# Kernel optimization log

Hardware: AMD Instinct MI355X
Metric: run time of the kernel (lower is better)

Reference implementation:

```python
import jax, jax.numpy as jnp
import numpy as np

ROWS, COLS = 4096, 8192
K = 4096                      # target_mask_size (<= COLS)
TEMPERATURE = 2.0 / 3.0


def setup_inputs() -> dict:
    key = jax.random.key(0)
    k1, k2 = jax.random.split(key)
    # param_init_fn: normal(mean=log(1-0.5)-log(0.5)=0, std=0.01)
    z_loga = jax.random.normal(k1, (ROWS, COLS), dtype=jnp.float32) * 0.01
    # eps = rand_like(...).clamp_(1e-6, 1-1e-6)
    eps = jax.random.uniform(k2, (ROWS, COLS), dtype=jnp.float32,
                             minval=1e-6, maxval=1.0 - 1e-6)
    return {"z_loga": z_loga, "eps": eps, "step": 0}


def reference(z_loga, eps, step):
    # Training branch of Mask.sample_z: gumbel-sigmoid + per-row top-k hard mask
    # with straight-through estimator.
    gumbel = -jnp.log(-jnp.log(eps))                       # [R, C]
    gumbel_mask = jax.nn.sigmoid((z_loga + gumbel) / TEMPERATURE)
    # per-row top-k hard selection (dim=1), scatter ones at top-k indices
    _, idx = jax.lax.top_k(gumbel_mask, K)                 # [R, K]
    rows = jnp.arange(gumbel_mask.shape[0])[:, None]       # [R, 1]
    hard = jnp.zeros_like(gumbel_mask).at[rows, idx].set(1.0)
    # straight-through: forward = hard, gradient flows through gumbel_mask
    st = hard - jax.lax.stop_gradient(gumbel_mask) + gumbel_mask
    return st.reshape(ROWS, COLS)                          # mask_output_shape
```

## Files before the change

kernel.cpp:

```cpp
#include <hip/hip_runtime.h>
#include <math.h>
#include <stdint.h>

#define ROWS 4096
#define COLS 8192
#define KSEL 4096
#define NT 256
#define NWAVE (NT / 64)
#define PT (COLS / (4 * NT))
#define NBINS 1024
#define WMAX 128
#define RANGE_HI 0.75f
#define LN2F 0.69314718056f

__device__ __forceinline__ int bin_of(float u) {
    int b = (int)(u * ((float)NBINS / RANGE_HI));
    b = b < 0 ? 0 : b;
    b = b > NBINS - 1 ? NBINS - 1 : b;
    return b;
}

__global__ __launch_bounds__(NT) void mask_topk_kernel(
    const float* __restrict__ z, const float* __restrict__ eps,
    float* __restrict__ out)
{
    __shared__ uint32_t hist[NWAVE][NBINS];
    __shared__ uint32_t wtot[NWAVE];
    __shared__ int      winIdx[WMAX];
    __shared__ uint32_t winSig[WMAX];
    __shared__ int      s_B, s_need2;
    __shared__ uint32_t s_wcount;

    const int row  = blockIdx.x;
    const int tid  = threadIdx.x;
    const int lane = tid & 63;
    const int wave = tid >> 6;
    const size_t rbase = (size_t)row * COLS;

    const float4* z4 = (const float4*)(z + rbase);
    const float4* e4 = (const float4*)(eps + rbase);
    float4 zr[PT], er[PT];
#pragma unroll
    for (int it = 0; it < PT; ++it) {
        zr[it] = z4[it * NT + tid];
        er[it] = e4[it * NT + tid];
    }

    for (int i = tid; i < NWAVE * NBINS; i += NT) ((uint32_t*)hist)[i] = 0;
    if (tid == 0) s_wcount = 0;
    __syncthreads();

    uint32_t cLo = 0, cHi = 0;
#pragma unroll
    for (int it = 0; it < PT; ++it) {
        float zz[4] = {zr[it].x, zr[it].y, zr[it].z, zr[it].w};
        float ee[4] = {er[it].x, er[it].y, er[it].z, er[it].w};
        float uu[4];
#pragma unroll
        for (int j = 0; j < 4; ++j) {
            float l1 = __builtin_amdgcn_logf(ee[j]) * LN2F;
            float l2 = __builtin_amdgcn_logf(-l1) * LN2F;
            uu[j] = zz[j] - l2;
            int b = bin_of(uu[j]);
            if (b == 0)              ++cLo;
            else if (b == NBINS - 1) ++cHi;
            else atomicAdd(&hist[wave][b], 1u);
        }
        zr[it].x = uu[0]; zr[it].y = uu[1]; zr[it].z = uu[2]; zr[it].w = uu[3];
    }
#pragma unroll
    for (int off = 32; off >= 1; off >>= 1) {
        cLo += __shfl_down(cLo, off, 64);
        cHi += __shfl_down(cHi, off, 64);
    }
    if (lane == 0) {
        atomicAdd(&hist[wave][0],         cLo);
        atomicAdd(&hist[wave][NBINS - 1], cHi);
    }
    __syncthreads();

    const int hb = tid * (NBINS / NT);
    uint32_t h[NBINS / NT];
    uint32_t cs = 0;
#pragma unroll
    for (int i = 0; i < NBINS / NT; ++i) {
        uint32_t t = 0;
#pragma unroll
        for (int c = 0; c < NWAVE; ++c) t += hist[c][hb + i];
        h[i] = t;
        cs += t;
    }
    uint32_t v = cs;
#pragma unroll
    for (int off = 1; off < 64; off <<= 1) {
        uint32_t t = __shfl_down(v, off, 64);
        if (lane + off < 64) v += t;
    }
    if (lane == 0) wtot[wave] = v;
    __syncthreads();
    uint32_t above = 0;
#pragma unroll
    for (int c = 0; c < NWAVE; ++c) above += (c > wave) ? wtot[c] : 0u;
    uint32_t cum = (v + above) - cs;

    for (int i = NBINS / NT - 1; i >= 0; --i) {
        if (cum < KSEL && KSEL <= cum + h[i]) {
            const int Bq = hb + i;
            uint32_t hB1 = 0;
            if (Bq + 1 < NBINS) {
#pragma unroll
                for (int c = 0; c < NWAVE; ++c) hB1 += hist[c][Bq + 1];
            }
            s_B = Bq;
            s_need2 = KSEL - (int)(cum - hB1);
        }
        cum += h[i];
    }
    __syncthreads();
    const int B = s_B;
    const int need2 = s_need2;

    float4* o4 = (float4*)(out + rbase);
#pragma unroll
    for (int it = 0; it < PT; ++it) {
        const int k = it * NT + tid;
        float uu[4] = {zr[it].x, zr[it].y, zr[it].z, zr[it].w};
        float oo[4];
#pragma unroll
        for (int j = 0; j < 4; ++j) {
            int b = bin_of(uu[j]);
            oo[j] = (b > B + 1) ? 1.0f : 0.0f;
            if (b >= B - 1 && b <= B + 1) {
                uint32_t slot = atomicAdd(&s_wcount, 1u);
                if (slot < WMAX) {
                    const int idx = k * 4 + j;
                    winIdx[slot] = idx;
                    float e   = eps[rbase + idx];
                    float zz  = z[rbase + idx];
                    float l1  = (float)log((double)e);
                    float l2  = (float)log((double)(-l1));
                    float g   = -l2;
                    float s   = zz + g;
                    float t   = s / (2.0f / 3.0f);
                    float ex  = (float)exp(-(double)t);
                    float sig = 1.0f / (1.0f + ex);
                    winSig[slot] = __float_as_uint(sig);
                }
            }
        }
        float4 ov; ov.x = oo[0]; ov.y = oo[1]; ov.z = oo[2]; ov.w = oo[3];
        o4[k] = ov;
    }
    __syncthreads();

    int w = (int)s_wcount; if (w > WMAX) w = WMAX;
    if (tid < 64) {
        for (int j = lane; j < w; j += 64) {
            uint32_t sj = winSig[j];
            int ij = winIdx[j];
            int rank = 0;
            for (int kk = 0; kk < w; ++kk) {
                uint32_t sk = winSig[kk];
                int ik = winIdx[kk];
                rank += (sk > sj || (sk == sj && ik < ij)) ? 1 : 0;
            }
            out[rbase + ij] = (rank < need2) ? 1.0f : 0.0f;
        }
    }
}

extern "C" void kernel_launch(void* const* d_in, const int* in_sizes, int n_in,
                              void* d_out, int out_size, void* d_ws, size_t ws_size,
                              hipStream_t stream) {
    const float* z   = (const float*)d_in[0];
    const float* eps = (const float*)d_in[1];
    float* out = (float*)d_out;
    hipLaunchKernelGGL(mask_topk_kernel, dim3(ROWS), dim3(NT), 0, stream,
                       z, eps, out);
}
```

Baseline: 322.8 us.

## Process one row per wavefront and keep packed bin indices in registers

```diff
diff --git a/kernel.cpp b/kernel.cpp
--- a/kernel.cpp
+++ b/kernel.cpp
@@ -7,11 +7,14 @@
 #define KSEL 4096
 #define NT 256
 #define NWAVE (NT / 64)
-#define PT (COLS / (4 * NT))
+#define NIT (COLS / (4 * 64))
 #define NBINS 1024
+#define BPL (NBINS / 64)
 #define WMAX 128
 #define RANGE_HI 0.75f
 #define LN2F 0.69314718056f
+
+typedef float fvec4 __attribute__((ext_vector_type(4)));
 
 __device__ __forceinline__ int bin_of(float u) {
     int b = (int)(u * ((float)NBINS / RANGE_HI));
@@ -20,53 +23,50 @@
     return b;
 }
 
-__global__ __launch_bounds__(NT) void mask_topk_kernel(
+__global__ __launch_bounds__(NT, 2) void mask_topk_kernel(
     const float* __restrict__ z, const float* __restrict__ eps,
     float* __restrict__ out)
 {
     __shared__ uint32_t hist[NWAVE][NBINS];
-    __shared__ uint32_t wtot[NWAVE];
-    __shared__ int      winIdx[WMAX];
-    __shared__ uint32_t winSig[WMAX];
-    __shared__ int      s_B, s_need2;
-    __shared__ uint32_t s_wcount;
+    __shared__ int      winIdx[NWAVE][WMAX];
+    __shared__ uint32_t winSig[NWAVE][WMAX];
+    __shared__ uint32_t wcnt[NWAVE];
+    __shared__ int      sB[NWAVE], sN2[NWAVE];
 
-    const int row  = blockIdx.x;
     const int tid  = threadIdx.x;
     const int lane = tid & 63;
     const int wave = tid >> 6;
+    const int row  = blockIdx.x * NWAVE + wave;
     const size_t rbase = (size_t)row * COLS;
 
-    const float4* z4 = (const float4*)(z + rbase);
-    const float4* e4 = (const float4*)(eps + rbase);
-    float4 zr[PT], er[PT];
 #pragma unroll
-    for (int it = 0; it < PT; ++it) {
-        zr[it] = z4[it * NT + tid];
-        er[it] = e4[it * NT + tid];
-    }
+    for (int i = 0; i < BPL; ++i) hist[wave][i * 64 + lane] = 0;
+    if (lane == 0) wcnt[wave] = 0;
 
-    for (int i = tid; i < NWAVE * NBINS; i += NT) ((uint32_t*)hist)[i] = 0;
-    if (tid == 0) s_wcount = 0;
-    __syncthreads();
-
+    const fvec4* z4 = (const fvec4*)(z + rbase);
+    const fvec4* e4 = (const fvec4*)(eps + rbase);
+    uint32_t pb[2 * NIT];
     uint32_t cLo = 0, cHi = 0;
 #pragma unroll
-    for (int it = 0; it < PT; ++it) {
-        float zz[4] = {zr[it].x, zr[it].y, zr[it].z, zr[it].w};
-        float ee[4] = {er[it].x, er[it].y, er[it].z, er[it].w};
-        float uu[4];
+    for (int it = 0; it < NIT; ++it) {
+        fvec4 zz4 = z4[it * 64 + lane];
+        fvec4 ee4 = e4[it * 64 + lane];
+        float zz[4] = {zz4.x, zz4.y, zz4.z, zz4.w};
+        float ee[4] = {ee4.x, ee4.y, ee4.z, ee4.w};
+        uint32_t bb[4];
 #pragma unroll
         for (int j = 0; j < 4; ++j) {
             float l1 = __builtin_amdgcn_logf(ee[j]) * LN2F;
             float l2 = __builtin_amdgcn_logf(-l1) * LN2F;
-            uu[j] = zz[j] - l2;
-            int b = bin_of(uu[j]);
+            float u  = zz[j] - l2;
+            int b = bin_of(u);
             if (b == 0)              ++cLo;
             else if (b == NBINS - 1) ++cHi;
             else atomicAdd(&hist[wave][b], 1u);
+            bb[j] = (uint32_t)b;
         }
-        zr[it].x = uu[0]; zr[it].y = uu[1]; zr[it].z = uu[2]; zr[it].w = uu[3];
+        pb[2 * it]     = bb[0] | (bb[1] << 16);
+        pb[2 * it + 1] = bb[2] | (bb[3] << 16);
     }
 #pragma unroll
     for (int off = 32; off >= 1; off >>= 1) {
@@ -77,18 +77,18 @@
         atomicAdd(&hist[wave][0],         cLo);
         atomicAdd(&hist[wave][NBINS - 1], cHi);
     }
-    __syncthreads();
+    asm volatile("s_waitcnt lgkmcnt(0)" ::: "memory");
 
-    const int hb = tid * (NBINS / NT);
-    uint32_t h[NBINS / NT];
-    uint32_t cs = 0;
+    uint32_t h[BPL]; uint32_t cs = 0;
+    {
+        const uint4* hv = (const uint4*)&hist[wave][lane * BPL];
 #pragma unroll
-    for (int i = 0; i < NBINS / NT; ++i) {
-        uint32_t t = 0;
-#pragma unroll
-        for (int c = 0; c < NWAVE; ++c) t += hist[c][hb + i];
-        h[i] = t;
-        cs += t;
+        for (int q = 0; q < BPL / 4; ++q) {
+            uint4 a = hv[q];
+            h[4 * q + 0] = a.x; h[4 * q + 1] = a.y;
+            h[4 * q + 2] = a.z; h[4 * q + 3] = a.w;
+            cs += a.x + a.y + a.z + a.w;
+        }
     }
     uint32_t v = cs;
 #pragma unroll
@@ -96,76 +96,67 @@
         uint32_t t = __shfl_down(v, off, 64);
         if (lane + off < 64) v += t;
     }
-    if (lane == 0) wtot[wave] = v;
-    __syncthreads();
-    uint32_t above = 0;
+    uint32_t cum = v - cs;
+    int Bc = -1, n2c = 0;
 #pragma unroll
-    for (int c = 0; c < NWAVE; ++c) above += (c > wave) ? wtot[c] : 0u;
-    uint32_t cum = (v + above) - cs;
-
-    for (int i = NBINS / NT - 1; i >= 0; --i) {
+    for (int i = BPL - 1; i >= 0; --i) {
         if (cum < KSEL && KSEL <= cum + h[i]) {
-            const int Bq = hb + i;
-            uint32_t hB1 = 0;
-            if (Bq + 1 < NBINS) {
-#pragma unroll
-                for (int c = 0; c < NWAVE; ++c) hB1 += hist[c][Bq + 1];
-            }
-            s_B = Bq;
-            s_need2 = KSEL - (int)(cum - hB1);
+            Bc = lane * BPL + i;
+            uint32_t hB1 = (Bc + 1 < NBINS) ? hist[wave][Bc + 1] : 0;
+            n2c = KSEL - (int)(cum - hB1);
         }
         cum += h[i];
     }
-    __syncthreads();
-    const int B = s_B;
-    const int need2 = s_need2;
+    if (Bc >= 0) { sB[wave] = Bc; sN2[wave] = n2c; }
+    asm volatile("s_waitcnt lgkmcnt(0)" ::: "memory");
+    const int B = sB[wave];
+    const int need2 = sN2[wave];
 
-    float4* o4 = (float4*)(out + rbase);
+    fvec4* o4 = (fvec4*)(out + rbase);
 #pragma unroll
-    for (int it = 0; it < PT; ++it) {
-        const int k = it * NT + tid;
-        float uu[4] = {zr[it].x, zr[it].y, zr[it].z, zr[it].w};
+    for (int it = 0; it < NIT; ++it) {
+        const int k = it * 64 + lane;
+        int bb[4] = { (int)(pb[2 * it] & 0xffffu), (int)(pb[2 * it] >> 16),
+                      (int)(pb[2 * it + 1] & 0xffffu), (int)(pb[2 * it + 1] >> 16) };
         float oo[4];
 #pragma unroll
         for (int j = 0; j < 4; ++j) {
-            int b = bin_of(uu[j]);
-            oo[j] = (b > B + 1) ? 1.0f : 0.0f;
-            if (b >= B - 1 && b <= B + 1) {
-                uint32_t slot = atomicAdd(&s_wcount, 1u);
-                if (slot < WMAX) {
-                    const int idx = k * 4 + j;
-                    winIdx[slot] = idx;
-                    float e   = eps[rbase + idx];
-                    float zz  = z[rbase + idx];
-                    float l1  = (float)log((double)e);
-                    float l2  = (float)log((double)(-l1));
-                    float g   = -l2;
-                    float s   = zz + g;
-                    float t   = s / (2.0f / 3.0f);
-                    float ex  = (float)exp(-(double)t);
-                    float sig = 1.0f / (1.0f + ex);
-                    winSig[slot] = __float_as_uint(sig);
-                }
+            oo[j] = (bb[j] > B + 1) ? 1.0f : 0.0f;
+            if (bb[j] >= B - 1 && bb[j] <= B + 1) {
+                uint32_t slot = atomicAdd(&wcnt[wave], 1u);
+                if (slot < WMAX) winIdx[wave][slot] = k * 4 + j;
             }
         }
-        float4 ov; ov.x = oo[0]; ov.y = oo[1]; ov.z = oo[2]; ov.w = oo[3];
+        fvec4 ov; ov.x = oo[0]; ov.y = oo[1]; ov.z = oo[2]; ov.w = oo[3];
         o4[k] = ov;
     }
-    __syncthreads();
 
-    int w = (int)s_wcount; if (w > WMAX) w = WMAX;
-    if (tid < 64) {
-        for (int j = lane; j < w; j += 64) {
-            uint32_t sj = winSig[j];
-            int ij = winIdx[j];
-            int rank = 0;
-            for (int kk = 0; kk < w; ++kk) {
-                uint32_t sk = winSig[kk];
-                int ik = winIdx[kk];
-                rank += (sk > sj || (sk == sj && ik < ij)) ? 1 : 0;
-            }
-            out[rbase + ij] = (rank < need2) ? 1.0f : 0.0f;
+    asm volatile("s_waitcnt lgkmcnt(0)" ::: "memory");
+    int wv = (int)wcnt[wave]; if (wv > WMAX) wv = WMAX;
+    for (int j = lane; j < wv; j += 64) {
+        int idx = winIdx[wave][j];
+        float e   = eps[rbase + idx];
+        float zz  = z[rbase + idx];
+        float l1  = (float)log((double)e);
+        float l2  = (float)log((double)(-l1));
+        float g   = -l2;
+        float s   = zz + g;
+        float t   = s / (2.0f / 3.0f);
+        float ex  = (float)exp(-(double)t);
+        float sig = 1.0f / (1.0f + ex);
+        winSig[wave][j] = __float_as_uint(sig);
+    }
+    asm volatile("s_waitcnt lgkmcnt(0) vmcnt(0)" ::: "memory");
+    for (int j = lane; j < wv; j += 64) {
+        uint32_t sj = winSig[wave][j];
+        int ij = winIdx[wave][j];
+        int rank = 0;
+        for (int kk = 0; kk < wv; ++kk) {
+            uint32_t sk = winSig[wave][kk];
+            int ik = winIdx[wave][kk];
+            rank += (sk > sj || (sk == sj && ik < ij)) ? 1 : 0;
         }
+        out[rbase + ij] = (rank < need2) ? 1.0f : 0.0f;
     }
 }
 
@@ -175,6 +166,6 @@
     const float* z   = (const float*)d_in[0];
     const float* eps = (const float*)d_in[1];
     float* out = (float*)d_out;
-    hipLaunchKernelGGL(mask_topk_kernel, dim3(ROWS), dim3(NT), 0, stream,
+    hipLaunchKernelGGL(mask_topk_kernel, dim3(ROWS / NWAVE), dim3(NT), 0, stream,
                        z, eps, out);
 }
```

Result: no change. 317.4 us (-1.7%).
